# Optimization experiments

Hardware: AMD Instinct MI355X
Metric: run time of the kernel (lower is better)

## Reference

```python
import jax, jax.numpy as jnp
import numpy as np

B, S, D = 1024, 200, 512
D_FF = 256


def setup_inputs() -> dict:
    key = jax.random.key(0)
    ks = jax.random.split(key, 8)
    s = 0.02  # init scale to keep gates in a sane range
    return {
        "target": jax.random.normal(ks[0], (B, D), jnp.float32),
        "history": jax.random.normal(ks[1], (B, S, D), jnp.float32),
        "W_ih": jax.random.normal(ks[2], (3 * D, D), jnp.float32) * s,
        "W_hh": jax.random.normal(ks[3], (3 * D, D), jnp.float32) * s,
        "b_ih": jnp.zeros((3 * D,), jnp.float32),
        "b_hh": jnp.zeros((3 * D,), jnp.float32),
        "W_fc": jax.random.normal(ks[4], (D_FF, 2 * D), jnp.float32) * s,
        "b_fc": jnp.zeros((D_FF,), jnp.float32),
        "W_sc": jax.random.normal(ks[5], (1, D_FF), jnp.float32) * s,
        "b_sc": jnp.zeros((1,), jnp.float32),
    }


def _gru(history, W_ih, W_hh, b_ih, b_hh):
    # Precompute input-side gate pre-activations for all steps: [B, S, 3D]
    gx = jnp.einsum("bsd,gd->bsg", history, W_ih) + b_ih
    d = history.shape[-1]
    h0 = jnp.zeros((history.shape[0], d), history.dtype)

    def step(h, gx_t):
        gh = h @ W_hh.T + b_hh  # [B, 3D]
        xr, xz, xn = jnp.split(gx_t, 3, axis=-1)
        hr, hz, hn = jnp.split(gh, 3, axis=-1)
        r = jax.nn.sigmoid(xr + hr)
        z = jax.nn.sigmoid(xz + hz)
        n = jnp.tanh(xn + r * hn)
        h_new = (1.0 - z) * n + z * h
        return h_new, h_new

    _, out = jax.lax.scan(step, h0, jnp.swapaxes(gx, 0, 1))  # out: [S, B, D]
    return jnp.swapaxes(out, 0, 1)  # [B, S, D]


def reference(target, history, W_ih, W_hh, b_ih, b_hh, W_fc, b_fc, W_sc, b_sc):
    d = target.shape[-1]
    gru_out = _gru(history, W_ih, W_hh, b_ih, b_hh)  # [B, S, D]

    # concat([gru_out, target]) @ W_fc.T  == gru_out @ Wg.T + target @ Wt.T
    Wg, Wt = W_fc[:, :d], W_fc[:, d:]
    pre = jnp.einsum("bsd,fd->bsf", gru_out, Wg) + (target @ Wt.T)[:, None, :] + b_fc
    hidden = jax.nn.gelu(pre, approximate=False)  # torch F.gelu default is exact erf
    scores = jnp.einsum("bsf,f->bs", hidden, W_sc[0]) + b_sc[0]  # [B, S]
    w = jax.nn.softmax(scores, axis=-1)
    interest = jnp.einsum("bs,bsd->bd", w, gru_out)  # [B, D]
    return jnp.concatenate([interest, target], axis=-1)  # [B, 2D]
```

## Files before the change

### kernel.cpp

```cpp
#include <hip/hip_runtime.h>

typedef __attribute__((ext_vector_type(8))) short short8v;
typedef __attribute__((ext_vector_type(4))) float f32x4;

#define NB 1024
#define NS 200
#define ND 512
#define NG 1536
#define NM 204800
#define NFF 256

#define GRU_P 4
#define GRU_G 64

__device__ __forceinline__ float bf2f(unsigned short u){
  union { unsigned u; float f; } v; v.u = ((unsigned)u) << 16; return v.f;
}
__device__ __forceinline__ unsigned short f2bf(float f){
  union { float f; unsigned u; } v; v.f = f;
  unsigned r = v.u + 0x7fffu + ((v.u >> 16) & 1u);
  return (unsigned short)(r >> 16);
}
__device__ __forceinline__ float sigm(float x){ return 1.f / (1.f + __expf(-x)); }
__device__ __forceinline__ float tanhfast(float x){ return 1.f - 2.f / (1.f + __expf(2.f * x)); }

__global__ void k_prepack(const float* __restrict__ W, unsigned short* __restrict__ out,
                          int ld, int coloff, int ntiles){
  int gid = blockIdx.x * 256 + threadIdx.x;
  if (gid >= ntiles * 1024) return;
  int ntile = gid >> 10; int rem = gid & 1023;
  int kk = rem >> 6; int lane = rem & 63;
  int c = ntile * 16 + (lane & 15);
  int k0 = kk * 32 + (lane >> 4) * 8;
  const float* s = W + (size_t)c * ld + coloff + k0;
  uint4 v;
  v.x = (unsigned)f2bf(s[0]) | ((unsigned)f2bf(s[1]) << 16);
  v.y = (unsigned)f2bf(s[2]) | ((unsigned)f2bf(s[3]) << 16);
  v.z = (unsigned)f2bf(s[4]) | ((unsigned)f2bf(s[5]) << 16);
  v.w = (unsigned)f2bf(s[6]) | ((unsigned)f2bf(s[7]) << 16);
  *(uint4*)(out + (size_t)gid * 8) = v;
}

__global__ void k_tvec(const float* __restrict__ target, const float* __restrict__ Wfc,
                       const float* __restrict__ bfc, float* __restrict__ tvec){
  __shared__ float tg[4][ND];
  int bb = blockIdx.x;
  int tid = threadIdx.x;
  for (int idx = tid; idx < 4 * ND; idx += 256){
    int j = idx >> 9, d = idx & 511;
    tg[j][d] = target[(size_t)(bb * 4 + j) * ND + d];
  }
  __syncthreads();
  const float* wrow = Wfc + (size_t)tid * 1024 + 512;
  float a0 = 0, a1 = 0, a2 = 0, a3 = 0;
  for (int d = 0; d < ND; ++d){
    float wv = wrow[d];
    a0 += tg[0][d] * wv; a1 += tg[1][d] * wv; a2 += tg[2][d] * wv; a3 += tg[3][d] * wv;
  }
  float bias = bfc[tid];
  tvec[(size_t)(bb * 4 + 0) * NFF + tid] = a0 + bias;
  tvec[(size_t)(bb * 4 + 1) * NFF + tid] = a1 + bias;
  tvec[(size_t)(bb * 4 + 2) * NFF + tid] = a2 + bias;
  tvec[(size_t)(bb * 4 + 3) * NFF + tid] = a3 + bias;
}

__global__ __launch_bounds__(256) void k_gemm_gx(const float* __restrict__ Af,
                                                 const unsigned short* __restrict__ Bpk,
                                                 const float* __restrict__ bih,
                                                 const float* __restrict__ bhh,
                                                 unsigned short* __restrict__ gx){
  __shared__ unsigned short As[128 * 64];
  int tid = threadIdx.x; int lane = tid & 63; int wid = tid >> 6;
  int wm = wid >> 1, wn = wid & 1;
  int Nb = blockIdx.x, Mb = blockIdx.y;
  const float* Abase = Af + (size_t)Mb * 128 * ND;
  const short8v* Bp = (const short8v*)Bpk;
  f32x4 acc[4][4];
  #pragma unroll
  for (int i = 0; i < 4; ++i)
    #pragma unroll
    for (int j = 0; j < 4; ++j) acc[i][j] = (f32x4){0.f, 0.f, 0.f, 0.f};

  for (int kc = 0; kc < 8; ++kc){
    __syncthreads();
    #pragma unroll
    for (int pass = 0; pass < 4; ++pass){
      int idx = pass * 256 + tid; int r = idx >> 3, ch = idx & 7;
      const float* src = Abase + (size_t)r * ND + kc * 64 + ch * 8;
      float4 f0 = *(const float4*)src;
      float4 f1 = *(const float4*)(src + 4);
      uint4 v;
      v.x = (unsigned)f2bf(f0.x) | ((unsigned)f2bf(f0.y) << 16);
      v.y = (unsigned)f2bf(f0.z) | ((unsigned)f2bf(f0.w) << 16);
      v.z = (unsigned)f2bf(f1.x) | ((unsigned)f2bf(f1.y) << 16);
      v.w = (unsigned)f2bf(f1.z) | ((unsigned)f2bf(f1.w) << 16);
      *(uint4*)&As[r * 64 + ch * 8] = v;
    }
    __syncthreads();
    #pragma unroll
    for (int i = 0; i < 2; ++i){
      short8v a[4];
      #pragma unroll
      for (int mt = 0; mt < 4; ++mt)
        a[mt] = *(const short8v*)&As[(wm * 64 + mt * 16 + (lane & 15)) * 64 + i * 32 + (lane >> 4) * 8];
      #pragma unroll
      for (int nt = 0; nt < 4; ++nt){
        short8v b = Bp[((size_t)(Nb * 8 + wn * 4 + nt) * 16 + (kc * 2 + i)) * 64 + lane];
        #pragma unroll
        for (int mt = 0; mt < 4; ++mt)
          acc[mt][nt] = __builtin_amdgcn_mfma_f32_16x16x32_bf16(a[mt], b, acc[mt][nt], 0, 0, 0);
      }
    }
  }
  #pragma unroll
  for (int mt = 0; mt < 4; ++mt){
    #pragma unroll
    for (int nt = 0; nt < 4; ++nt){
      int gcol = Nb * 128 + wn * 64 + nt * 16 + (lane & 15);
      float bv = bih[gcol] + (gcol < 1024 ? bhh[gcol] : 0.f);
      #pragma unroll
      for (int r = 0; r < 4; ++r){
        int grow = Mb * 128 + wm * 64 + mt * 16 + (lane >> 4) * 4 + r;
        gx[(size_t)grow * NG + gcol] = f2bf(acc[mt][nt][r] + bv);
      }
    }
  }
}

__global__ __launch_bounds__(512, 1) void k_gru9(const unsigned short* __restrict__ gx,
                                                 const unsigned short* __restrict__ Wpk,
                                                 const float* __restrict__ bhh,
                                                 unsigned short* __restrict__ gout,
                                                 unsigned long long* __restrict__ hx,
                                                 int* __restrict__ flags){
  __shared__ unsigned short hbuf[2][16 * 512];
  __shared__ unsigned short hstg[16][136];
  int tid = threadIdx.x; int lane = tid & 63; int nh = tid >> 6;
  int bid = blockIdx.x; int g = bid & 63; int s = bid >> 6;
  int colg = lane & 15;
  int rowg = lane >> 4;
  int c_h = s * 128 + nh * 16 + colg;
  int b0 = g * 16;
  int* gfl = flags + g * 32;

  for (int i = tid; i < 16 * 512; i += 512) hbuf[0][i] = 0;

  short8v wf[3][16];
  const short8v* Wp = (const short8v*)Wpk;
  #pragma unroll
  for (int gg = 0; gg < 3; ++gg){
    int ntile = gg * 32 + s * 8 + nh;
    #pragma unroll
    for (int kk = 0; kk < 16; ++kk)
      wf[gg][kk] = Wp[((size_t)ntile * 16 + kk) * 64 + lane];
  }
  float bN = bhh[1024 + c_h];
  float hreg[4] = {0.f, 0.f, 0.f, 0.f};

  int wpair = (nh & 3) * 2;
  const unsigned long long* f1 = (const unsigned long long*)&gfl[(nh >> 2) * 8 + wpair];
  const unsigned long long* f2 = (const unsigned long long*)&gfl[((nh >> 2) + 2) * 8 + wpair];

  unsigned short cxr[4], cxz[4], cxn[4];
  #pragma unroll
  for (int r = 0; r < 4; ++r){
    const unsigned short* gp = gx + ((size_t)(b0 + rowg * 4 + r) * NS + 0) * NG;
    cxr[r] = gp[c_h]; cxz[r] = gp[512 + c_h]; cxn[r] = gp[1024 + c_h];
  }
  __syncthreads();

  #pragma unroll 1
  for (int t = 0; t < NS; ++t){
    int par = t & 1;
    const unsigned short* hr = hbuf[par];
    f32x4 acc0 = (f32x4){0.f,0.f,0.f,0.f}, acc1 = acc0, acc2 = acc0;
    #pragma unroll
    for (int kc = 0; kc < 16; ++kc){
      short8v a = *(const short8v*)&hr[kc * 512 + lane * 8];
      acc0 = __builtin_amdgcn_mfma_f32_16x16x32_bf16(a, wf[0][kc], acc0, 0, 0, 0);
      acc1 = __builtin_amdgcn_mfma_f32_16x16x32_bf16(a, wf[1][kc], acc1, 0, 0, 0);
      acc2 = __builtin_amdgcn_mfma_f32_16x16x32_bf16(a, wf[2][kc], acc2, 0, 0, 0);
    }
    unsigned short hnew[4];
    #pragma unroll
    for (int r = 0; r < 4; ++r){
      float rr = sigm(bf2f(cxr[r]) + acc0[r]);
      float zz = sigm(bf2f(cxz[r]) + acc1[r]);
      float nn = tanhfast(bf2f(cxn[r]) + rr * (acc2[r] + bN));
      float h = nn + zz * (hreg[r] - nn);
      hreg[r] = h;
      hnew[r] = f2bf(h);
    }

    if (t + 1 < NS){
      unsigned long long* hxp = hx + (size_t)par * (1024 * 128);
      #pragma unroll
      for (int r = 0; r < 4; ++r) hstg[rowg * 4 + r][nh * 16 + colg] = hnew[r];
      asm volatile("s_waitcnt lgkmcnt(0)" ::: "memory");
      {
        unsigned long long v8 = *(const unsigned long long*)&hstg[lane & 15][nh * 16 + (lane >> 4) * 4];
        __hip_atomic_store(&hxp[(size_t)(b0 + (lane & 15)) * 128 + s * 32 + nh * 4 + (lane >> 4)], v8,
                           __ATOMIC_RELAXED, __HIP_MEMORY_SCOPE_AGENT);
      }
      asm volatile("s_waitcnt vmcnt(0)" ::: "memory");
      if (lane == 0)
        __hip_atomic_store(&gfl[s * 8 + nh], t + 1, __ATOMIC_RELAXED, __HIP_MEMORY_SCOPE_AGENT);
      #pragma unroll
      for (int r = 0; r < 4; ++r)
        gout[((size_t)(b0 + rowg * 4 + r) * NS + t) * ND + c_h] = hnew[r];
      #pragma unroll
      for (int r = 0; r < 4; ++r){
        const unsigned short* gp = gx + ((size_t)(b0 + rowg * 4 + r) * NS + (t + 1)) * NG;
        cxr[r] = gp[c_h]; cxz[r] = gp[512 + c_h]; cxn[r] = gp[1024 + c_h];
      }
      int need = t + 1;
      unsigned long long fa;
      do {
        fa = __hip_atomic_load(f1, __ATOMIC_RELAXED, __HIP_MEMORY_SCOPE_AGENT);
      } while ((int)(fa & 0xffffffffu) < need || (int)(fa >> 32) < need);
      asm volatile("" ::: "memory");
      size_t base1 = (size_t)(b0 + (lane & 15)) * 128 + nh * 8 + (lane >> 4) * 2;
      unsigned long long u0 = __hip_atomic_load(&hxp[base1],     __ATOMIC_RELAXED, __HIP_MEMORY_SCOPE_AGENT);
      unsigned long long u1 = __hip_atomic_load(&hxp[base1 + 1], __ATOMIC_RELAXED, __HIP_MEMORY_SCOPE_AGENT);
      do {
        fa = __hip_atomic_load(f2, __ATOMIC_RELAXED, __HIP_MEMORY_SCOPE_AGENT);
      } while ((int)(fa & 0xffffffffu) < need || (int)(fa >> 32) < need);
      asm volatile("" ::: "memory");
      size_t base2 = base1 + 64;
      unsigned long long u2 = __hip_atomic_load(&hxp[base2],     __ATOMIC_RELAXED, __HIP_MEMORY_SCOPE_AGENT);
      unsigned long long u3 = __hip_atomic_load(&hxp[base2 + 1], __ATOMIC_RELAXED, __HIP_MEMORY_SCOPE_AGENT);
      unsigned short* hw = hbuf[par ^ 1];
      { unsigned long long tmp[2] = {u0, u1}; *(uint4*)&hw[nh * 512 + lane * 8] = *(const uint4*)tmp; }
      { unsigned long long tmp[2] = {u2, u3}; *(uint4*)&hw[(nh + 8) * 512 + lane * 8] = *(const uint4*)tmp; }
      __syncthreads();
    } else {
      #pragma unroll
      for (int r = 0; r < 4; ++r)
        gout[((size_t)(b0 + rowg * 4 + r) * NS + t) * ND + c_h] = hnew[r];
    }
  }
}

__global__ __launch_bounds__(512) void k_gemm_s4(const unsigned short* __restrict__ A,
                                                 const unsigned short* __restrict__ Bpk,
                                                 const float* __restrict__ tvec,
                                                 const float* __restrict__ Wsc,
                                                 const float* __restrict__ bsc,
                                                 float* __restrict__ scores){
  __shared__ unsigned short As[128 * 64];
  __shared__ float spart[4][128];
  int tid = threadIdx.x; int lane = tid & 63; int wid = tid >> 6;
  int wm = wid >> 2, wn = wid & 3;
  int Mb = blockIdx.x;
  const unsigned short* Abase = A + (size_t)Mb * 128 * ND;
  const short8v* Bp = (const short8v*)Bpk;
  f32x4 acc[4][4];
  #pragma unroll
  for (int i = 0; i < 4; ++i)
    #pragma unroll
    for (int j = 0; j < 4; ++j) acc[i][j] = (f32x4){0.f, 0.f, 0.f, 0.f};

  for (int kc = 0; kc < 8; ++kc){
    __syncthreads();
    #pragma unroll
    for (int pass = 0; pass < 2; ++pass){
      int idx = pass * 512 + tid; int r = idx >> 3, ch = idx & 7;
      uint4 v = *(const uint4*)(Abase + (size_t)r * ND + kc * 64 + ch * 8);
      *(uint4*)&As[r * 64 + ch * 8] = v;
    }
    __syncthreads();
    #pragma unroll
    for (int i = 0; i < 2; ++i){
      short8v a[4];
      #pragma unroll
      for (int mt = 0; mt < 4; ++mt)
        a[mt] = *(const short8v*)&As[(wm * 64 + mt * 16 + (lane & 15)) * 64 + i * 32 + (lane >> 4) * 8];
      #pragma unroll
      for (int nt = 0; nt < 4; ++nt){
        short8v b = Bp[((size_t)(wn * 4 + nt) * 16 + (kc * 2 + i)) * 64 + lane];
        #pragma unroll
        for (int mt = 0; mt < 4; ++mt)
          acc[mt][nt] = __builtin_amdgcn_mfma_f32_16x16x32_bf16(a[mt], b, acc[mt][nt], 0, 0, 0);
      }
    }
  }
  #pragma unroll
  for (int mt = 0; mt < 4; ++mt){
    #pragma unroll
    for (int r = 0; r < 4; ++r){
      int rowl = wm * 64 + mt * 16 + (lane >> 4) * 4 + r;
      unsigned grow = (unsigned)(Mb * 128 + rowl);
      unsigned bidx = grow / 200u;
      float rowsum = 0.f;
      #pragma unroll
      for (int nt = 0; nt < 4; ++nt){
        int gcol = wn * 64 + nt * 16 + (lane & 15);
        float pre = acc[mt][nt][r] + tvec[(size_t)bidx * NFF + gcol];
        float g = 0.5f * pre * (1.f + erff(pre * 0.70710678118654752f));
        rowsum += g * Wsc[gcol];
      }
      rowsum += __shfl_xor(rowsum, 1, 64);
      rowsum += __shfl_xor(rowsum, 2, 64);
      rowsum += __shfl_xor(rowsum, 4, 64);
      rowsum += __shfl_xor(rowsum, 8, 64);
      if ((lane & 15) == 0) spart[wn][rowl] = rowsum;
    }
  }
  __syncthreads();
  if (tid < 128){
    float s = spart[0][tid] + spart[1][tid] + spart[2][tid] + spart[3][tid] + bsc[0];
    scores[(size_t)Mb * 128 + tid] = s;
  }
}

__global__ void k_out(const float* __restrict__ scores, const unsigned short* __restrict__ gout,
                      const float* __restrict__ target, float* __restrict__ out){
  int b = blockIdx.x; int tid = threadIdx.x;
  __shared__ float sw[NS];
  __shared__ float red[4];
  float v = (tid < NS) ? scores[(size_t)b * NS + tid] : -3.0e38f;
  float m = v;
  #pragma unroll
  for (int off = 32; off >= 1; off >>= 1) m = fmaxf(m, __shfl_xor(m, off, 64));
  if ((tid & 63) == 0) red[tid >> 6] = m;
  __syncthreads();
  m = fmaxf(fmaxf(red[0], red[1]), fmaxf(red[2], red[3]));
  float e = (tid < NS) ? __expf(v - m) : 0.f;
  if (tid < NS) sw[tid] = e;
  float su = e;
  #pragma unroll
  for (int off = 32; off >= 1; off >>= 1) su += __shfl_xor(su, off, 64);
  __syncthreads();
  if ((tid & 63) == 0) red[tid >> 6] = su;
  __syncthreads();
  float inv = 1.f / (red[0] + red[1] + red[2] + red[3]);
  int d0 = tid * 2;
  float a0 = 0.f, a1 = 0.f;
  const unsigned short* gbase = gout + (size_t)b * NS * ND + d0;
  for (int s = 0; s < NS; ++s){
    unsigned u = *(const unsigned*)(gbase + (size_t)s * ND);
    float wgt = sw[s];
    a0 += wgt * bf2f((unsigned short)(u & 0xffffu));
    a1 += wgt * bf2f((unsigned short)(u >> 16));
  }
  out[(size_t)b * 1024 + d0] = a0 * inv;
  out[(size_t)b * 1024 + d0 + 1] = a1 * inv;
  float2 tv = *(const float2*)(target + (size_t)b * ND + d0);
  out[(size_t)b * 1024 + 512 + d0] = tv.x;
  out[(size_t)b * 1024 + 512 + d0 + 1] = tv.y;
}

extern "C" void kernel_launch(void* const* d_in, const int* in_sizes, int n_in,
                              void* d_out, int out_size, void* d_ws, size_t ws_size,
                              hipStream_t stream) {
  const float* target  = (const float*)d_in[0];
  const float* history = (const float*)d_in[1];
  const float* W_ih    = (const float*)d_in[2];
  const float* W_hh    = (const float*)d_in[3];
  const float* b_ih    = (const float*)d_in[4];
  const float* b_hh    = (const float*)d_in[5];
  const float* W_fc    = (const float*)d_in[6];
  const float* b_fc    = (const float*)d_in[7];
  const float* W_sc    = (const float*)d_in[8];
  const float* b_sc    = (const float*)d_in[9];

  char* ws = (char*)d_ws;
  size_t off = 0;
  unsigned short* gx     = (unsigned short*)(ws + off); off += 629145600ull;
  unsigned short* gout   = (unsigned short*)(ws + off); off += 209715200ull;
  unsigned short* wih_pk = (unsigned short*)(ws + off); off += 1572864ull;
  unsigned short* whh_pk = (unsigned short*)(ws + off); off += 1572864ull;
  unsigned short* wg_pk  = (unsigned short*)(ws + off); off += 262144ull;
  float*          tvec   = (float*)(ws + off);          off += 1048576ull;
  float*          scores = (float*)(ws + off);          off += 819200ull;
  unsigned long long* hx = (unsigned long long*)(ws + off); off += 2097152ull;
  int*            flags  = (int*)(ws + off);             off += 8192ull;
  if (ws_size < off) return;
  float* outp = (float*)d_out;

  (void)hipMemsetAsync(flags, 0, GRU_G * 32 * sizeof(int), stream);
  k_prepack<<<384, 256, 0, stream>>>(W_ih, wih_pk, 512, 0, 96);
  k_prepack<<<384, 256, 0, stream>>>(W_hh, whh_pk, 512, 0, 96);
  k_prepack<<<64, 256, 0, stream>>>(W_fc, wg_pk, 1024, 0, 16);
  k_tvec<<<256, 256, 0, stream>>>(target, W_fc, b_fc, tvec);
  k_gemm_gx<<<dim3(12, 1600), 256, 0, stream>>>(history, wih_pk, b_ih, b_hh, gx);
  k_gru9<<<256, 512, 0, stream>>>(gx, whh_pk, b_hh, gout, hx, flags);
  k_gemm_s4<<<1600, 512, 0, stream>>>(gout, wg_pk, tvec, W_sc, b_sc, scores);
  k_out<<<1024, 256, 0, stream>>>(scores, gout, target, outp);
}
```

Measured before the change: 2.352 ms.

## Prefetch next-step gate inputs and merge GRU flag waits into one wave poll

The next timestep's precomputed input gates are now loaded from global memory at the top of each step, so their latency hides behind the MFMA recurrence instead of sitting on the critical path after the exchange. The two sequential flag spins on 64-bit flag pairs are replaced by a single wave-wide poll of all 32 flags using __all, followed by all four hidden-state loads issued together. The gout store moves after those loads are issued. The per-wave staging buffer is padded differently to cut LDS conflicts. Waiting on all flags adds extra polling traffic, and the prefetch holds more registers.

New measurement: 2.540 ms. 8.0% more time.

```diff
diff --git a/kernel.cpp b/kernel.cpp
--- a/kernel.cpp
+++ b/kernel.cpp
@@ -127,14 +127,14 @@
   }
 }
 
-__global__ __launch_bounds__(512, 1) void k_gru9(const unsigned short* __restrict__ gx,
-                                                 const unsigned short* __restrict__ Wpk,
-                                                 const float* __restrict__ bhh,
-                                                 unsigned short* __restrict__ gout,
-                                                 unsigned long long* __restrict__ hx,
-                                                 int* __restrict__ flags){
+__global__ __launch_bounds__(512, 1) void k_gru10(const unsigned short* __restrict__ gx,
+                                                  const unsigned short* __restrict__ Wpk,
+                                                  const float* __restrict__ bhh,
+                                                  unsigned short* __restrict__ gout,
+                                                  unsigned long long* __restrict__ hx,
+                                                  int* __restrict__ flags){
   __shared__ unsigned short hbuf[2][16 * 512];
-  __shared__ unsigned short hstg[16][136];
+  __shared__ unsigned short hstg[8][16][20];
   int tid = threadIdx.x; int lane = tid & 63; int nh = tid >> 6;
   int bid = blockIdx.x; int g = bid & 63; int s = bid >> 6;
   int colg = lane & 15;
@@ -157,10 +157,6 @@
   float bN = bhh[1024 + c_h];
   float hreg[4] = {0.f, 0.f, 0.f, 0.f};
 
-  int wpair = (nh & 3) * 2;
-  const unsigned long long* f1 = (const unsigned long long*)&gfl[(nh >> 2) * 8 + wpair];
-  const unsigned long long* f2 = (const unsigned long long*)&gfl[((nh >> 2) + 2) * 8 + wpair];
-
   unsigned short cxr[4], cxz[4], cxn[4];
   #pragma unroll
   for (int r = 0; r < 4; ++r){
@@ -173,6 +169,14 @@
   for (int t = 0; t < NS; ++t){
     int par = t & 1;
     const unsigned short* hr = hbuf[par];
+    unsigned short nxr[4], nxz[4], nxn[4];
+    if (t + 1 < NS){
+      #pragma unroll
+      for (int r = 0; r < 4; ++r){
+        const unsigned short* gp = gx + ((size_t)(b0 + rowg * 4 + r) * NS + (t + 1)) * NG;
+        nxr[r] = gp[c_h]; nxz[r] = gp[512 + c_h]; nxn[r] = gp[1024 + c_h];
+      }
+    }
     f32x4 acc0 = (f32x4){0.f,0.f,0.f,0.f}, acc1 = acc0, acc2 = acc0;
     #pragma unroll
     for (int kc = 0; kc < 16; ++kc){
@@ -195,40 +199,31 @@
     if (t + 1 < NS){
       unsigned long long* hxp = hx + (size_t)par * (1024 * 128);
       #pragma unroll
-      for (int r = 0; r < 4; ++r) hstg[rowg * 4 + r][nh * 16 + colg] = hnew[r];
+      for (int r = 0; r < 4; ++r) hstg[nh][rowg * 4 + r][colg] = hnew[r];
       asm volatile("s_waitcnt lgkmcnt(0)" ::: "memory");
       {
-        unsigned long long v8 = *(const unsigned long long*)&hstg[lane & 15][nh * 16 + (lane >> 4) * 4];
+        unsigned long long v8 = *(const unsigned long long*)&hstg[nh][lane & 15][(lane >> 4) * 4];
         __hip_atomic_store(&hxp[(size_t)(b0 + (lane & 15)) * 128 + s * 32 + nh * 4 + (lane >> 4)], v8,
                            __ATOMIC_RELAXED, __HIP_MEMORY_SCOPE_AGENT);
       }
       asm volatile("s_waitcnt vmcnt(0)" ::: "memory");
       if (lane == 0)
         __hip_atomic_store(&gfl[s * 8 + nh], t + 1, __ATOMIC_RELAXED, __HIP_MEMORY_SCOPE_AGENT);
+      {
+        int need = t + 1; int fv;
+        do {
+          fv = (lane < 32) ? __hip_atomic_load(&gfl[lane], __ATOMIC_RELAXED, __HIP_MEMORY_SCOPE_AGENT) : need;
+        } while (!__all(fv >= need));
+      }
+      asm volatile("" ::: "memory");
+      size_t base1 = (size_t)(b0 + (lane & 15)) * 128 + nh * 8 + (lane >> 4) * 2;
+      unsigned long long u0 = __hip_atomic_load(&hxp[base1],      __ATOMIC_RELAXED, __HIP_MEMORY_SCOPE_AGENT);
+      unsigned long long u1 = __hip_atomic_load(&hxp[base1 + 1],  __ATOMIC_RELAXED, __HIP_MEMORY_SCOPE_AGENT);
+      unsigned long long u2 = __hip_atomic_load(&hxp[base1 + 64], __ATOMIC_RELAXED, __HIP_MEMORY_SCOPE_AGENT);
+      unsigned long long u3 = __hip_atomic_load(&hxp[base1 + 65], __ATOMIC_RELAXED, __HIP_MEMORY_SCOPE_AGENT);
       #pragma unroll
       for (int r = 0; r < 4; ++r)
         gout[((size_t)(b0 + rowg * 4 + r) * NS + t) * ND + c_h] = hnew[r];
-      #pragma unroll
-      for (int r = 0; r < 4; ++r){
-        const unsigned short* gp = gx + ((size_t)(b0 + rowg * 4 + r) * NS + (t + 1)) * NG;
-        cxr[r] = gp[c_h]; cxz[r] = gp[512 + c_h]; cxn[r] = gp[1024 + c_h];
-      }
-      int need = t + 1;
-      unsigned long long fa;
-      do {
-        fa = __hip_atomic_load(f1, __ATOMIC_RELAXED, __HIP_MEMORY_SCOPE_AGENT);
-      } while ((int)(fa & 0xffffffffu) < need || (int)(fa >> 32) < need);
-      asm volatile("" ::: "memory");
-      size_t base1 = (size_t)(b0 + (lane & 15)) * 128 + nh * 8 + (lane >> 4) * 2;
-      unsigned long long u0 = __hip_atomic_load(&hxp[base1],     __ATOMIC_RELAXED, __HIP_MEMORY_SCOPE_AGENT);
-      unsigned long long u1 = __hip_atomic_load(&hxp[base1 + 1], __ATOMIC_RELAXED, __HIP_MEMORY_SCOPE_AGENT);
-      do {
-        fa = __hip_atomic_load(f2, __ATOMIC_RELAXED, __HIP_MEMORY_SCOPE_AGENT);
-      } while ((int)(fa & 0xffffffffu) < need || (int)(fa >> 32) < need);
-      asm volatile("" ::: "memory");
-      size_t base2 = base1 + 64;
-      unsigned long long u2 = __hip_atomic_load(&hxp[base2],     __ATOMIC_RELAXED, __HIP_MEMORY_SCOPE_AGENT);
-      unsigned long long u3 = __hip_atomic_load(&hxp[base2 + 1], __ATOMIC_RELAXED, __HIP_MEMORY_SCOPE_AGENT);
       unsigned short* hw = hbuf[par ^ 1];
       { unsigned long long tmp[2] = {u0, u1}; *(uint4*)&hw[nh * 512 + lane * 8] = *(const uint4*)tmp; }
       { unsigned long long tmp[2] = {u2, u3}; *(uint4*)&hw[(nh + 8) * 512 + lane * 8] = *(const uint4*)tmp; }
@@ -238,6 +233,8 @@
       for (int r = 0; r < 4; ++r)
         gout[((size_t)(b0 + rowg * 4 + r) * NS + t) * ND + c_h] = hnew[r];
     }
+    #pragma unroll
+    for (int r = 0; r < 4; ++r){ cxr[r] = nxr[r]; cxz[r] = nxz[r]; cxn[r] = nxn[r]; }
   }
 }
 
@@ -384,7 +381,7 @@
   k_prepack<<<64, 256, 0, stream>>>(W_fc, wg_pk, 1024, 0, 16);
   k_tvec<<<256, 256, 0, stream>>>(target, W_fc, b_fc, tvec);
   k_gemm_gx<<<dim3(12, 1600), 256, 0, stream>>>(history, wih_pk, b_ih, b_hh, gx);
-  k_gru9<<<256, 512, 0, stream>>>(gx, whh_pk, b_hh, gout, hx, flags);
+  k_gru10<<<256, 512, 0, stream>>>(gx, whh_pk, b_hh, gout, hx, flags);
   k_gemm_s4<<<1600, 512, 0, stream>>>(gout, wg_pk, tvec, W_sc, b_sc, scores);
   k_out<<<1024, 256, 0, stream>>>(scores, gout, target, outp);
 }
```
